# Performance work log

Measured on AMD Instinct MI355X. Metric: run time of the kernel, lower is better.

The kernel has to match this reference:

```python
import jax, jax.numpy as jnp
import numpy as np

B, N, C = 8, 1024, 768
H = 12
D = C // H  # head_dim = 64
SCALE = D ** -0.5


def setup_inputs() -> dict:
    key = jax.random.key(0)
    k1, k2, k3 = jax.random.split(key, 3)
    x = jax.random.normal(k1, (B, N, C), dtype=jnp.float32)
    # nn.Linear(dim, 3*dim, bias=False): weight [3C, C]
    w_qkv = jax.random.normal(k2, (3 * C, C), dtype=jnp.float32) * (C ** -0.5)
    # nn.Linear(dim, dim): weight [C, C], bias [C]
    w_proj = jax.random.normal(k3, (C, C), dtype=jnp.float32) * (C ** -0.5)
    b_proj = jnp.zeros((C,), dtype=jnp.float32)
    return {"x": x, "w_qkv": w_qkv, "w_proj": w_proj, "b_proj": b_proj}


def reference(x, w_qkv, w_proj, b_proj):
    b, n, c = x.shape
    # qkv projection: [B,N,3C] -> [3,B,H,N,D]
    qkv = jnp.einsum('bnc,fc->bnf', x, w_qkv)
    qkv = qkv.reshape(b, n, 3, H, D).transpose(2, 0, 3, 1, 4)
    q, k, v = qkv[0], qkv[1], qkv[2]
    # scaled dot-product attention (q scaled as in timm: q @ k^T * scale)
    attn = jnp.einsum('bhnd,bhmd->bhnm', q, k) * SCALE
    attn = jax.nn.softmax(attn, axis=-1)
    out = jnp.einsum('bhnm,bhmd->bhnd', attn, v)  # [B,H,N,D]
    out = out.transpose(0, 2, 1, 3).reshape(b, n, c)
    # output projection
    out = jnp.einsum('bnc,oc->bno', out, w_proj) + b_proj
    return out
```

## Files before the change

### kernel.cpp

```cpp
#include <hip/hip_runtime.h>
#include <hip/hip_bf16.h>
#include <stdint.h>


typedef unsigned short u16;
typedef __attribute__((ext_vector_type(8))) short    short8;
typedef __attribute__((ext_vector_type(4))) short    short4v;
typedef __attribute__((ext_vector_type(8))) __bf16   bf16x8;
typedef __attribute__((ext_vector_type(8))) unsigned short ushort8_t;
typedef __attribute__((ext_vector_type(4))) float    f32x4;

#define QSCALE 0.18033688011112042f

__device__ __forceinline__ u16 f2bf(float f) {
  union { float f; uint32_t u; } v; v.f = f;
  uint32_t u = v.u;
  u += 0x7fffu + ((u >> 16) & 1u);
  return (u16)(u >> 16);
}

__device__ __forceinline__ uint32_t pack_bf16(float hi, float lo) {
  uint32_t a = __builtin_bit_cast(uint32_t, hi) + 0x8000u;
  uint32_t b = __builtin_bit_cast(uint32_t, lo) + 0x8000u;
  return __builtin_amdgcn_perm(a, b, 0x07060302u);
}

__device__ __forceinline__ uint32_t pack_trunc(float hi, float lo) {
  return __builtin_amdgcn_perm(__builtin_bit_cast(uint32_t, hi),
                               __builtin_bit_cast(uint32_t, lo), 0x07060302u);
}

__device__ __forceinline__ float fast_exp2(float x) {
#if __has_builtin(__builtin_amdgcn_exp2f)
  return __builtin_amdgcn_exp2f(x);
#else
  float r;
  asm("v_exp_f32 %0, %1" : "=v"(r) : "v"(x));
  return r;
#endif
}

__device__ __forceinline__ void gl_lds16(const void* g, void* l) {
  __builtin_amdgcn_global_load_lds(
      (const __attribute__((address_space(1))) void*)g,
      (__attribute__((address_space(3))) void*)l, 16, 0, 0);
}

__device__ __forceinline__ f32x4 mfma16(short8 a, short8 b, f32x4 c) {
  return __builtin_amdgcn_mfma_f32_16x16x32_bf16(
      __builtin_bit_cast(bf16x8, a), __builtin_bit_cast(bf16x8, b), c, 0, 0, 0);
}

__device__ __forceinline__ f32x4 mfma16k16(short4v a, short4v b, f32x4 c) {
#if __has_builtin(__builtin_amdgcn_mfma_f32_16x16x16bf16_1k)
  return __builtin_amdgcn_mfma_f32_16x16x16bf16_1k(a, b, c, 0, 0, 0);
#else
  f32x4 d = c;
  asm volatile("v_mfma_f32_16x16x16_bf16 %0, %1, %2, %0"
               : "+v"(d) : "v"(a), "v"(b));
  return d;
#endif
}

__global__ void cvt3_kernel(const float* __restrict__ x, const float* __restrict__ wq,
                            const float* __restrict__ wp, u16* __restrict__ dst) {
  const int i = blockIdx.x * blockDim.x + threadIdx.x;
  constexpr int NX = 6291456 / 4, NQ = 1769472 / 4, NP = 589824 / 4;
  float4 v;
  if (i < NX)                v = ((const float4*)x)[i];
  else if (i < NX + NQ)      v = ((const float4*)wq)[i - NX];
  else if (i < NX + NQ + NP) v = ((const float4*)wp)[i - NX - NQ];
  else return;
  ushort4 o;
  o.x = f2bf(v.x); o.y = f2bf(v.y); o.z = f2bf(v.z); o.w = f2bf(v.w);
  ((ushort4*)dst)[i] = o;
}

template <int NBX, int MODE, int BN>
__global__ __launch_bounds__(256)
void gemm_bt(const u16* __restrict__ A, const u16* __restrict__ Bw,
             u16* __restrict__ Qb, u16* __restrict__ Kb, u16* __restrict__ Vtb,
             float* __restrict__ outF, const float* __restrict__ bias) {
  constexpr int K = 768;
  constexpr int NIT = K / 32;
  constexpr int MB = (BN == 128) ? 4 : 2;
  constexpr int SL = 2 + BN / 64;
  __shared__ union {
    struct { alignas(16) u16 A[3][128 * 32]; alignas(16) u16 B[3][BN * 32]; } st;
    alignas(16) u16 vx[4][64 * 40];
  } sm;
  const int t = threadIdx.x;
  const int lane = t & 63;
  const int w = t >> 6;
  const int col = lane & 15;
  const int quad = lane >> 4;
  const int lin = blockIdx.x;
  const int xcd = lin & 7, j = lin >> 3;
  const int mi = xcd * 8 + (j & 7);
  const int ni = j >> 3;
  const int m0 = mi * 128;
  const int n0 = ni * BN;
  const int wm = (BN == 128) ? (w >> 1) * 64 : w * 32;
  const int wn = (BN == 128) ? (w & 1) * 64 : 0;

  f32x4 acc[MB][4];
#pragma unroll
  for (int i = 0; i < MB; i++)
#pragma unroll
    for (int jj = 0; jj < 4; jj++) acc[i][jj] = (f32x4){0.f, 0.f, 0.f, 0.f};

  auto stage = [&](int buf, int k0) {
#pragma unroll
    for (int i = 0; i < 2; i++) {
      const int c = t + i * 256;
      const int row = c >> 2, kc = c & 3;
      gl_lds16(A + (m0 + row) * K + k0 + kc * 8, &sm.st.A[buf][c * 8]);
    }
#pragma unroll
    for (int i = 0; i < BN / 64; i++) {
      const int c = t + i * 256;
      const int row = c >> 2, kc = c & 3;
      gl_lds16(Bw + (n0 + row) * K + k0 + kc * 8, &sm.st.B[buf][c * 8]);
    }
  };

  stage(0, 0);
  stage(1, 32);
  for (int it = 0; it < NIT; it++) {
    const int buf = it % 3;
    if (it < NIT - 1)
      asm volatile("s_waitcnt vmcnt(%0) lgkmcnt(0)" :: "n"(SL) : "memory");
    else
      asm volatile("s_waitcnt vmcnt(0) lgkmcnt(0)" ::: "memory");
    __builtin_amdgcn_s_barrier();
    __builtin_amdgcn_sched_barrier(0);
    if (it + 2 < NIT) stage((it + 2) % 3, (it + 2) * 32);
    short8 af[MB], bf[4];
#pragma unroll
    for (int mb = 0; mb < MB; mb++)
      af[mb] = *(const short8*)&sm.st.A[buf][(wm + mb * 16 + col) * 32 + quad * 8];
#pragma unroll
    for (int nb = 0; nb < 4; nb++)
      bf[nb] = *(const short8*)&sm.st.B[buf][(wn + nb * 16 + col) * 32 + quad * 8];
#pragma unroll
    for (int mb = 0; mb < MB; mb++)
#pragma unroll
      for (int nb = 0; nb < 4; nb++)
        acc[mb][nb] = mfma16(af[mb], bf[nb], acc[mb][nb]);
  }

  if (MODE == 0) {
    const int tsel = n0 / 768;
    if (tsel == 2) {
      __syncthreads();
      u16* vx = sm.vx[w];
      const int b = (m0 + wm) >> 10;
      const int h = (n0 + wn - 1536) >> 6;
      const int nbase = ((m0 + wm) & 1023);
#pragma unroll
      for (int p = 0; p < 2; p++) {
#pragma unroll
        for (int mh = 0; mh < 2; mh++) {
          const int mb = p * 2 + mh;
#pragma unroll
          for (int nb = 0; nb < 4; nb++) {
            const int dloc = nb * 16 + col;
            const int tl = mh * 16 + quad * 4;
            uint2 pk;
            pk.x = pack_bf16(acc[mb][nb][1], acc[mb][nb][0]);
            pk.y = pack_bf16(acc[mb][nb][3], acc[mb][nb][2]);
            *(uint2*)&vx[dloc * 40 + tl] = pk;
          }
        }
        asm volatile("s_waitcnt lgkmcnt(0)" ::: "memory");
#pragma unroll
        for (int i = 0; i < 4; i++) {
          const int dloc = i * 16 + (lane >> 2);
          const int tl = (lane & 3) * 8;
          ushort8_t v = *(const ushort8_t*)&vx[dloc * 40 + tl];
          *(ushort8_t*)&Vtb[((b * 12 + h) * 64 + dloc) * 1024 + nbase + p * 32 + tl] = v;
        }
      }
    } else {
      u16* dst = (tsel == 0) ? Qb : Kb;
      const float scale = (tsel == 0) ? QSCALE : 1.0f;
#pragma unroll
      for (int mb = 0; mb < MB; mb++)
#pragma unroll
        for (int nb = 0; nb < 4; nb++)
#pragma unroll
          for (int r = 0; r < 4; r++) {
            const int row = m0 + wm + mb * 16 + quad * 4 + r;
            const int cc = n0 + wn + nb * 16 + col;
            const int b = row >> 10, n = row & 1023;
            const int hd = cc - tsel * 768;
            const int h = hd >> 6, d = hd & 63;
            dst[((b * 12 + h) * 1024 + n) * 64 + d] = f2bf(acc[mb][nb][r] * scale);
          }
    }
  } else {
#pragma unroll
    for (int mb = 0; mb < MB; mb++)
#pragma unroll
      for (int nb = 0; nb < 4; nb++)
#pragma unroll
        for (int r = 0; r < 4; r++) {
          const int row = m0 + wm + mb * 16 + quad * 4 + r;
          const int cc = n0 + wn + nb * 16 + col;
          outF[(size_t)row * 768 + cc] = acc[mb][nb][r] + bias[cc];
        }
  }
}

__global__ __launch_bounds__(256, 3)
void attn_kernel(const u16* __restrict__ Qb, const u16* __restrict__ Kb,
                 const u16* __restrict__ Vtb, u16* __restrict__ attnb) {
  __shared__ alignas(16) u16 Ks[3][64 * 64];
  __shared__ alignas(16) u16 Vs[3][64 * 64];
  const int t = threadIdx.x;
  const int lane = t & 63;
  const int w = t >> 6;
  const int col = lane & 15;
  const int quad = lane >> 4;
  const int lin = blockIdx.x;
  const int xcd = lin & 7, idx = lin >> 3;
  const int bh = xcd * 12 + idx % 12;
  const int qt = idx / 12;

  const u16* Qh = Qb + bh * 65536;
  const u16* Kh = Kb + bh * 65536;
  const u16* Vh = Vtb + bh * 65536;

  const int qrow0 = qt * 128 + w * 32;
  short8 qf[2][2];
#pragma unroll
  for (int g = 0; g < 2; g++)
#pragma unroll
    for (int s = 0; s < 2; s++)
      qf[g][s] = *(const short8*)&Qh[(qrow0 + g * 16 + col) * 64 + s * 32 + quad * 8];

  f32x4 oaccT[2][4];
#pragma unroll
  for (int g = 0; g < 2; g++)
#pragma unroll
    for (int nb = 0; nb < 4; nb++) oaccT[g][nb] = (f32x4){0.f, 0.f, 0.f, 0.f};
  f32x4 lsum[2];
  lsum[0] = (f32x4){0.f, 0.f, 0.f, 0.f};
  lsum[1] = (f32x4){0.f, 0.f, 0.f, 0.f};
  const short4v onesf = {0x3F80, 0x3F80, 0x3F80, 0x3F80};

  auto stage = [&](int buf, int kt) {
#pragma unroll
    for (int i = 0; i < 2; i++) {
      const int c = t + i * 256;
      const int row = c >> 3, jj = c & 7;
      const int js = jj ^ (row & 7);
      gl_lds16(Kh + (kt * 64 + row) * 64 + js * 8, &Ks[buf][c * 8]);
      gl_lds16(Vh + row * 1024 + kt * 64 + js * 8, &Vs[buf][c * 8]);
    }
  };

  stage(0, 0);
  stage(1, 1);
  for (int kt = 0; kt < 16; kt++) {
    const int buf = kt % 3;
    if (kt < 15)
      asm volatile("s_waitcnt vmcnt(4) lgkmcnt(0)" ::: "memory");
    else
      asm volatile("s_waitcnt vmcnt(0) lgkmcnt(0)" ::: "memory");
    __builtin_amdgcn_s_barrier();
    __builtin_amdgcn_sched_barrier(0);
    if (kt + 2 < 16) stage((kt + 2) % 3, kt + 2);

    f32x4 sv[2][4];
#pragma unroll
    for (int g = 0; g < 2; g++)
#pragma unroll
      for (int kb = 0; kb < 4; kb++) sv[g][kb] = (f32x4){0.f, 0.f, 0.f, 0.f};
#pragma unroll
    for (int kb = 0; kb < 4; kb++) {
      const int key = kb * 16 + col;
#pragma unroll
      for (int s = 0; s < 2; s++) {
        const short8 kf = *(const short8*)&Ks[buf][key * 64 + ((s * 4 + quad) ^ (key & 7)) * 8];
        sv[0][kb] = mfma16(kf, qf[0][s], sv[0][kb]);
        sv[1][kb] = mfma16(kf, qf[1][s], sv[1][kb]);
      }
    }

    short4v pfrag[2][4];
#pragma unroll
    for (int g = 0; g < 2; g++) {
#pragma unroll
      for (int kb = 0; kb < 4; kb++) {
        const float p0 = fast_exp2(sv[g][kb][0]);
        const float p1 = fast_exp2(sv[g][kb][1]);
        const float p2 = fast_exp2(sv[g][kb][2]);
        const float p3 = fast_exp2(sv[g][kb][3]);
        uint2 pk = {pack_trunc(p1, p0), pack_trunc(p3, p2)};
        pfrag[g][kb] = __builtin_bit_cast(short4v, pk);
        lsum[g] = mfma16k16(onesf, pfrag[g][kb], lsum[g]);
      }
    }

#pragma unroll
    for (int nb = 0; nb < 4; nb++) {
      const int d = nb * 16 + col;
#pragma unroll
      for (int kb = 0; kb < 4; kb++) {
        const int chunk = kb * 2 + (quad >> 1);
        const short4v vf = *(const short4v*)
            &Vs[buf][d * 64 + ((chunk ^ (d & 7)) * 8) + (quad & 1) * 4];
        oaccT[0][nb] = mfma16k16(vf, pfrag[0][kb], oaccT[0][nb]);
        oaccT[1][nb] = mfma16k16(vf, pfrag[1][kb], oaccT[1][nb]);
      }
    }
  }

  const int b = bh / 12, h = bh % 12;
#pragma unroll
  for (int g = 0; g < 2; g++) {
    const float inv = 1.0f / lsum[g][0];
    const int n = qrow0 + g * 16 + col;
#pragma unroll
    for (int nb = 0; nb < 4; nb++) {
      const int cc = h * 64 + nb * 16 + quad * 4;
      uint2 pk;
      pk.x = pack_bf16(oaccT[g][nb][1] * inv, oaccT[g][nb][0] * inv);
      pk.y = pack_bf16(oaccT[g][nb][3] * inv, oaccT[g][nb][2] * inv);
      *(uint2*)&attnb[(b * 1024 + n) * 768 + cc] = pk;
    }
  }
}

extern "C" void kernel_launch(void* const* d_in, const int* in_sizes, int n_in,
                              void* d_out, int out_size, void* d_ws, size_t ws_size,
                              hipStream_t stream) {
  const float* x      = (const float*)d_in[0];
  const float* w_qkv  = (const float*)d_in[1];
  const float* w_proj = (const float*)d_in[2];
  const float* b_proj = (const float*)d_in[3];
  float* out = (float*)d_out;
  char* ws = (char*)d_ws;

  u16* xb    = (u16*)(ws + 0);
  u16* wqb   = (u16*)(ws + 12582912);
  u16* wpb   = (u16*)(ws + 16121856);
  u16* Qb    = (u16*)(ws + 17301504);
  u16* Kb    = (u16*)(ws + 29884416);
  u16* Vtb   = (u16*)(ws + 42467328);
  u16* attnb = (u16*)(ws + 0);

  cvt3_kernel<<<8448, 256, 0, stream>>>(x, w_qkv, w_proj, xb);
  gemm_bt<18, 0, 128><<<1152, 256, 0, stream>>>(xb, wqb, Qb, Kb, Vtb, nullptr, nullptr);
  attn_kernel<<<768, 256, 0, stream>>>(Qb, Kb, Vtb, attnb);
  gemm_bt<12, 1, 64><<<768, 256, 0, stream>>>(attnb, wpb, nullptr, nullptr, nullptr, out, b_proj);
}
```

Measured before the change: 111.0 us.

## Fuse fp32-to-bf16 conversion of x into QKV GEMM A-tile loading

```diff
diff --git a/kernel.cpp b/kernel.cpp
--- a/kernel.cpp
+++ b/kernel.cpp
@@ -62,14 +62,13 @@
 #endif
 }
 
-__global__ void cvt3_kernel(const float* __restrict__ x, const float* __restrict__ wq,
+__global__ void cvt3_kernel(const float* __restrict__ wq,
                             const float* __restrict__ wp, u16* __restrict__ dst) {
   const int i = blockIdx.x * blockDim.x + threadIdx.x;
-  constexpr int NX = 6291456 / 4, NQ = 1769472 / 4, NP = 589824 / 4;
+  constexpr int NQ = 1769472 / 4, NP = 589824 / 4;
   float4 v;
-  if (i < NX)                v = ((const float4*)x)[i];
-  else if (i < NX + NQ)      v = ((const float4*)wq)[i - NX];
-  else if (i < NX + NQ + NP) v = ((const float4*)wp)[i - NX - NQ];
+  if (i < NQ)           v = ((const float4*)wq)[i];
+  else if (i < NQ + NP) v = ((const float4*)wp)[i - NQ];
   else return;
   ushort4 o;
   o.x = f2bf(v.x); o.y = f2bf(v.y); o.z = f2bf(v.z); o.w = f2bf(v.w);
@@ -78,13 +77,13 @@
 
 template <int NBX, int MODE, int BN>
 __global__ __launch_bounds__(256)
-void gemm_bt(const u16* __restrict__ A, const u16* __restrict__ Bw,
+void gemm_bt(const float* __restrict__ Ax, const u16* __restrict__ A,
+             const u16* __restrict__ Bw,
              u16* __restrict__ Qb, u16* __restrict__ Kb, u16* __restrict__ Vtb,
              float* __restrict__ outF, const float* __restrict__ bias) {
   constexpr int K = 768;
   constexpr int NIT = K / 32;
   constexpr int MB = (BN == 128) ? 4 : 2;
-  constexpr int SL = 2 + BN / 64;
   __shared__ union {
     struct { alignas(16) u16 A[3][128 * 32]; alignas(16) u16 B[3][BN * 32]; } st;
     alignas(16) u16 vx[4][64 * 40];
@@ -109,13 +108,7 @@
 #pragma unroll
     for (int jj = 0; jj < 4; jj++) acc[i][jj] = (f32x4){0.f, 0.f, 0.f, 0.f};
 
-  auto stage = [&](int buf, int k0) {
-#pragma unroll
-    for (int i = 0; i < 2; i++) {
-      const int c = t + i * 256;
-      const int row = c >> 2, kc = c & 3;
-      gl_lds16(A + (m0 + row) * K + k0 + kc * 8, &sm.st.A[buf][c * 8]);
-    }
+  auto stageB = [&](int buf, int k0) {
 #pragma unroll
     for (int i = 0; i < BN / 64; i++) {
       const int c = t + i * 256;
@@ -124,29 +117,94 @@
     }
   };
 
-  stage(0, 0);
-  stage(1, 32);
-  for (int it = 0; it < NIT; it++) {
-    const int buf = it % 3;
-    if (it < NIT - 1)
-      asm volatile("s_waitcnt vmcnt(%0) lgkmcnt(0)" :: "n"(SL) : "memory");
-    else
-      asm volatile("s_waitcnt vmcnt(0) lgkmcnt(0)" ::: "memory");
-    __builtin_amdgcn_s_barrier();
-    __builtin_amdgcn_sched_barrier(0);
-    if (it + 2 < NIT) stage((it + 2) % 3, (it + 2) * 32);
-    short8 af[MB], bf[4];
-#pragma unroll
-    for (int mb = 0; mb < MB; mb++)
-      af[mb] = *(const short8*)&sm.st.A[buf][(wm + mb * 16 + col) * 32 + quad * 8];
-#pragma unroll
-    for (int nb = 0; nb < 4; nb++)
-      bf[nb] = *(const short8*)&sm.st.B[buf][(wn + nb * 16 + col) * 32 + quad * 8];
-#pragma unroll
-    for (int mb = 0; mb < MB; mb++)
+  if constexpr (MODE == 0) {
+    const int arow = t >> 1, ahalf = t & 1;
+    const float* abase = Ax + (size_t)(m0 + arow) * K + ahalf * 16;
+    float4 areg[4];
+    auto loadA = [&](int k0) {
+#pragma unroll
+      for (int i = 0; i < 4; i++)
+        areg[i] = ((const float4*)(abase + k0))[i];
+    };
+    auto writeA = [&](int buf) {
+      uint4 q0, q1;
+      q0.x = pack_bf16(areg[0].y, areg[0].x); q0.y = pack_bf16(areg[0].w, areg[0].z);
+      q0.z = pack_bf16(areg[1].y, areg[1].x); q0.w = pack_bf16(areg[1].w, areg[1].z);
+      q1.x = pack_bf16(areg[2].y, areg[2].x); q1.y = pack_bf16(areg[2].w, areg[2].z);
+      q1.z = pack_bf16(areg[3].y, areg[3].x); q1.w = pack_bf16(areg[3].w, areg[3].z);
+      *(uint4*)&sm.st.A[buf][arow * 32 + ahalf * 16] = q0;
+      *(uint4*)&sm.st.A[buf][arow * 32 + ahalf * 16 + 8] = q1;
+    };
+    loadA(0);
+    stageB(0, 0);
+    asm volatile("s_waitcnt vmcnt(2)" ::: "memory");
+    writeA(0);
+    loadA(32);
+    stageB(1, 32);
+    for (int it = 0; it < NIT; it++) {
+      const int buf = it % 3;
+      if (it < NIT - 1)
+        asm volatile("s_waitcnt vmcnt(6) lgkmcnt(0)" ::: "memory");
+      else
+        asm volatile("s_waitcnt vmcnt(0) lgkmcnt(0)" ::: "memory");
+      __builtin_amdgcn_s_barrier();
+      __builtin_amdgcn_sched_barrier(0);
+      if (it < NIT - 1) {
+        asm volatile("s_waitcnt vmcnt(2)" ::: "memory");
+        writeA((it + 1) % 3);
+        if (it < NIT - 2) {
+          loadA((it + 2) * 32);
+          stageB((it + 2) % 3, (it + 2) * 32);
+        }
+      }
+      short8 af[MB], bf[4];
+#pragma unroll
+      for (int mb = 0; mb < MB; mb++)
+        af[mb] = *(const short8*)&sm.st.A[buf][(wm + mb * 16 + col) * 32 + quad * 8];
 #pragma unroll
       for (int nb = 0; nb < 4; nb++)
-        acc[mb][nb] = mfma16(af[mb], bf[nb], acc[mb][nb]);
+        bf[nb] = *(const short8*)&sm.st.B[buf][(wn + nb * 16 + col) * 32 + quad * 8];
+#pragma unroll
+      for (int mb = 0; mb < MB; mb++)
+#pragma unroll
+        for (int nb = 0; nb < 4; nb++)
+          acc[mb][nb] = mfma16(af[mb], bf[nb], acc[mb][nb]);
+    }
+  } else {
+    constexpr int SL = 2 + BN / 64;
+    auto stage = [&](int buf, int k0) {
+#pragma unroll
+      for (int i = 0; i < 2; i++) {
+        const int c = t + i * 256;
+        const int row = c >> 2, kc = c & 3;
+        gl_lds16(A + (m0 + row) * K + k0 + kc * 8, &sm.st.A[buf][c * 8]);
+      }
+      stageB(buf, k0);
+    };
+    stage(0, 0);
+    stage(1, 32);
+    for (int it = 0; it < NIT; it++) {
+      const int buf = it % 3;
+      if (it < NIT - 1)
+        asm volatile("s_waitcnt vmcnt(%0) lgkmcnt(0)" :: "n"(SL) : "memory");
+      else
+        asm volatile("s_waitcnt vmcnt(0) lgkmcnt(0)" ::: "memory");
+      __builtin_amdgcn_s_barrier();
+      __builtin_amdgcn_sched_barrier(0);
+      if (it + 2 < NIT) stage((it + 2) % 3, (it + 2) * 32);
+      short8 af[MB], bf[4];
+#pragma unroll
+      for (int mb = 0; mb < MB; mb++)
+        af[mb] = *(const short8*)&sm.st.A[buf][(wm + mb * 16 + col) * 32 + quad * 8];
+#pragma unroll
+      for (int nb = 0; nb < 4; nb++)
+        bf[nb] = *(const short8*)&sm.st.B[buf][(wn + nb * 16 + col) * 32 + quad * 8];
+#pragma unroll
+      for (int mb = 0; mb < MB; mb++)
+#pragma unroll
+        for (int nb = 0; nb < 4; nb++)
+          acc[mb][nb] = mfma16(af[mb], bf[nb], acc[mb][nb]);
+    }
   }
 
   if (MODE == 0) {
@@ -343,7 +401,6 @@
   float* out = (float*)d_out;
   char* ws = (char*)d_ws;
 
-  u16* xb    = (u16*)(ws + 0);
   u16* wqb   = (u16*)(ws + 12582912);
   u16* wpb   = (u16*)(ws + 16121856);
   u16* Qb    = (u16*)(ws + 17301504);
@@ -351,8 +408,8 @@
   u16* Vtb   = (u16*)(ws + 42467328);
   u16* attnb = (u16*)(ws + 0);
 
-  cvt3_kernel<<<8448, 256, 0, stream>>>(x, w_qkv, w_proj, xb);
-  gemm_bt<18, 0, 128><<<1152, 256, 0, stream>>>(xb, wqb, Qb, Kb, Vtb, nullptr, nullptr);
+  cvt3_kernel<<<2304, 256, 0, stream>>>(w_qkv, w_proj, wqb);
+  gemm_bt<18, 0, 128><<<1152, 256, 0, stream>>>(x, nullptr, wqb, Qb, Kb, Vtb, nullptr, nullptr);
   attn_kernel<<<768, 256, 0, stream>>>(Qb, Kb, Vtb, attnb);
-  gemm_bt<12, 1, 64><<<768, 256, 0, stream>>>(attnb, wpb, nullptr, nullptr, nullptr, out, b_proj);
-}
+  gemm_bt<12, 1, 64><<<768, 256, 0, stream>>>(nullptr, attnb, wpb, nullptr, nullptr, nullptr, out, b_proj);
+}
```

Measured after the change: 114.5 us. +3.1%, slower.
